# Performance work log

Measured on AMD Instinct MI355X. Metric: run time of the kernel, lower is better.

Reference implementation:

```python
import jax, jax.numpy as jnp
import numpy as np

B, C_IN, C_OUT, RANK, MODES, N = 32, 64, 64, 16, 64, 8192


def setup_inputs() -> dict:
    key = jax.random.key(0)
    k0, k1, k2, k3, k4 = jax.random.split(key, 5)
    x = jax.random.normal(k0, (B, C_IN, N), dtype=jnp.float32)
    U_r = jax.random.normal(k1, (C_IN, RANK), dtype=jnp.float32)
    U_i = jax.random.normal(k2, (C_IN, RANK), dtype=jnp.float32)
    V_r = jax.random.normal(k3, (RANK, C_OUT), dtype=jnp.float32)
    V_i = jax.random.normal(k4, (RANK, C_OUT), dtype=jnp.float32)
    S = jnp.ones((RANK,), dtype=jnp.float32)
    return {"x": x, "U_r": U_r, "U_i": U_i, "V_r": V_r, "V_i": V_i, "S": S}


def reference(x, U_r, U_i, V_r, V_i, S):
    # rFFT over spatial dim, orthonormal normalization (matches torch norm='ortho')
    x_fft = jnp.fft.rfft(x, axis=-1, norm='ortho')          # [B, C_in, N//2+1] complex
    n_freq = x_fft.shape[-1]
    modes = min(MODES, n_freq)
    x_modes = x_fft[..., :modes]                             # [B, C_in, modes]

    U = U_r + 1j * U_i                                       # [C_in, rank]
    V = V_r + 1j * V_i                                       # [rank, C_out]
    # w = (U * S) @ V, then slice first `modes` output channels (as in source)
    w = jnp.einsum('ir,ro->io', U * S[None, :].astype(U.dtype), V)
    w = w[..., :modes]                                       # no-op when C_out == modes

    out_modes = jnp.einsum('bix,io->box', x_modes, w)        # [B, C_out, modes]
    # zero-fill remaining spectrum (equivalent to zeros_like + slice assign)
    full = jnp.pad(out_modes, ((0, 0), (0, 0), (0, n_freq - modes)))
    return jnp.fft.irfft(full, n=x.shape[-1], axis=-1, norm='ortho')
```

## Files before the change

### kernel.cpp

```cpp
#include <hip/hip_runtime.h>

#define NPTS   8192
#define BATCH  32
#define CIN    64
#define COUT   64
#define RANKK  16
#define ROWS   (BATCH * CIN)
#define KB_SPLIT 16

typedef _Float16 f16;
typedef _Float16 f16x4 __attribute__((ext_vector_type(4)));
typedef _Float16 f16x8 __attribute__((ext_vector_type(8)));
typedef float    f32x4 __attribute__((ext_vector_type(4)));

__device__ __forceinline__ void gload16(const void* g, void* l) {
  __builtin_amdgcn_global_load_lds(
      (const __attribute__((address_space(1))) void*)g,
      (__attribute__((address_space(3))) void*)l, 16, 0, 0);
}

__global__ __launch_bounds__(256) void build_tables(f16* __restrict__ T,
                                                    f16* __restrict__ Tt) {
  __shared__ f16 tile[128][18];
  const int n0 = blockIdx.x * 16;
  const int t = threadIdx.x;
#pragma unroll
  for (int j = 0; j < 8; ++j) {
    int flat = t + 256 * j;
    int c = flat >> 4, dn = flat & 15;
    int k = c & 63, n = n0 + dn;
    int m = (k * n) & (NPTS - 1);
    float ang = (float)m * (6.28318530717958647692f / (float)NPTS);
    float sv, cv;
    sincosf(ang, &sv, &cv);
    tile[c][dn] = (f16)((c < 64) ? cv : sv);
  }
  __syncthreads();
#pragma unroll
  for (int j = 0; j < 8; ++j) {
    int flat = t + 256 * j;
    int c = flat >> 4, dn = flat & 15;
    f16 v = tile[c][dn];
    f16 vm = ((c & 1) ? (f16)(-v) : v);
    T[(size_t)c * NPTS + n0 + dn] = v;
    T[(size_t)c * NPTS + n0 + dn + NPTS / 2] = vm;
  }
#pragma unroll
  for (int j = 0; j < 8; ++j) {
    int flat = t + 256 * j;
    int dn = flat >> 7, c = flat & 127;
    f16 v = tile[c][dn];
    f16 vm = ((c & 1) ? (f16)(-v) : v);
    Tt[(size_t)(n0 + dn) * 128 + c] = v;
    Tt[(size_t)(n0 + dn + NPTS / 2) * 128 + c] = vm;
  }
}

__global__ __launch_bounds__(512) void fwd_dft(const float* __restrict__ x,
                                               const f16* __restrict__ T,
                                               f16* __restrict__ Sp) {
  __shared__ __align__(16) char lds[3 * 16384];
  const int t    = threadIdx.x;
  const int w    = t >> 6;
  const int lane = t & 63;
  const int rl = lane & 15, hi = lane >> 4;
  const int kb = blockIdx.x & (KB_SPLIT - 1);
  const int r0 = (blockIdx.x >> 4) * 64;
  const int k0 = kb * (NPTS / KB_SPLIT);

  const int xr_ = t >> 3;
  const int xo_ = ((t & 7) ^ (xr_ & 7)) << 2;
  const int tr_ = t >> 2;
  const int to_ = ((t & 3) ^ (tr_ & 3)) << 3;
  const float* xs0 = x + (size_t)(r0 + xr_) * NPTS + k0 + xo_;
  const f16*   ts0 = T + (size_t)tr_ * NPTS + k0 + to_;
  const int wu = w * 1024;

  auto STAGE = [&](int kt, int slot) {
    char* xb = lds + slot * 16384;
    char* tb = xb + 8192;
    const int kk = kt * 32;
    gload16(xs0 + kk, xb + wu);
    gload16(ts0 + kk, tb + wu);
  };

  f32x4 acc[4];
#pragma unroll
  for (int i = 0; i < 4; ++i) acc[i] = (f32x4){0.f, 0.f, 0.f, 0.f};

  const int h  = w >> 1;
  const int cg = w & 1;
  const int axr = h * 16 + rl;
  const int ad0 = (axr * 8 + ((2 * hi) ^ (axr & 7))) * 16;
  const int ad1 = (axr * 8 + ((2 * hi + 1) ^ (axr & 7))) * 16;
  int bd[4];
#pragma unroll
  for (int s = 0; s < 4; ++s) {
    int trow = cg * 64 + s * 16 + rl;
    bd[s] = (trow * 4 + (hi ^ (trow & 3))) * 16;
  }

  auto COMPUTE = [&](int slot) {
    char* xb = lds + slot * 16384;
    char* tb = xb + 8192;
    f32x4 a0 = *(const f32x4*)(xb + ad0);
    f32x4 a1 = *(const f32x4*)(xb + ad1);
    f16x8 af;
#pragma unroll
    for (int j = 0; j < 4; ++j) { af[j] = (f16)a0[j]; af[4 + j] = (f16)a1[j]; }
#pragma unroll
    for (int s = 0; s < 4; ++s) {
      f16x8 bf = *(const f16x8*)(tb + bd[s]);
      acc[s] = __builtin_amdgcn_mfma_f32_16x16x32_f16(af, bf, acc[s], 0, 0, 0);
    }
  };

  STAGE(0, 0);
  STAGE(1, 1);
  asm volatile("s_waitcnt vmcnt(2)" ::: "memory");
  __builtin_amdgcn_s_barrier();

  int sc = 0, ss = 2;
  for (int kt = 0; kt < 16; ++kt) {
    if (kt + 2 < 16) STAGE(kt + 2, ss);
    COMPUTE(sc);
    if (kt < 15) {
      if (kt + 2 < 16)
        asm volatile("s_waitcnt vmcnt(2)" ::: "memory");
      else
        asm volatile("s_waitcnt vmcnt(0)" ::: "memory");
      __builtin_amdgcn_s_barrier();
    }
    sc = (sc == 2) ? 0 : sc + 1;
    ss = (ss == 2) ? 0 : ss + 1;
  }

  f16* out = Sp + ((size_t)kb * ROWS + r0 + h * 16) * 128 + cg * 64;
#pragma unroll
  for (int s = 0; s < 4; ++s)
#pragma unroll
    for (int i = 0; i < 4; ++i)
      out[(hi * 4 + i) * 128 + s * 16 + rl] = (f16)acc[s][i];
}

__global__ __launch_bounds__(256) void reduce_k(const f16* __restrict__ Sp,
                                                float* __restrict__ Sred) {
  const int idx = blockIdx.x * 256 + threadIdx.x;
  const f16x4* src = (const f16x4*)Sp;
  f32x4 acc = (f32x4){0.f, 0.f, 0.f, 0.f};
#pragma unroll
  for (int s = 0; s < KB_SPLIT; ++s) {
    f16x4 v = src[(size_t)s * (ROWS * 128 / 4) + idx];
#pragma unroll
    for (int e = 0; e < 4; ++e) acc[e] += (float)v[e];
  }
  ((f32x4*)Sred)[idx] = acc;
}

__global__ __launch_bounds__(256) void mix3(const float* __restrict__ Sred,
                                            const float* __restrict__ Ur,
                                            const float* __restrict__ Ui,
                                            const float* __restrict__ Vr,
                                            const float* __restrict__ Vi,
                                            const float* __restrict__ Sv,
                                            f16* __restrict__ Qh) {
  __shared__ float Srs[64][64], Sis[64][64];
  __shared__ float wr_s[64][4], wi_s[64][4];
  const int b  = blockIdx.x >> 4;
  const int og = blockIdx.x & 15;
  const int t  = threadIdx.x;

#pragma unroll
  for (int j = 0; j < 8; ++j) {
    int f4 = t + 256 * j;
    int i = f4 >> 5, kc = (f4 & 31) * 4;
    f32x4 v = *(const f32x4*)(Sred + ((size_t)(b * 64 + i)) * 128 + kc);
    if (kc < 64) *(f32x4*)&Srs[i][kc] = v;
    else         *(f32x4*)&Sis[i][kc - 64] = v;
  }

  {
    int i = t >> 2, ol = t & 3, o = og * 4 + ol;
    float wr = 0.f, wi = 0.f;
#pragma unroll
    for (int r = 0; r < RANKK; ++r) {
      float ur = Ur[i * RANKK + r], ui = Ui[i * RANKK + r];
      float vr = Vr[r * COUT + o],  vi = Vi[r * COUT + o];
      float s = Sv[r];
      wr += s * (ur * vr - ui * vi);
      wi += s * (ur * vi + ui * vr);
    }
    wr_s[i][ol] = wr;
    wi_s[i][ol] = wi;
  }
  __syncthreads();

  const int ol = t >> 6, k = t & 63, o = og * 4 + ol;
  float qr = 0.f, qi = 0.f;
#pragma unroll 4
  for (int i = 0; i < 64; ++i) {
    float sr = Srs[i][k], si = Sis[i][k];
    float wr = wr_s[i][ol], wi = wi_s[i][ol];
    qr += sr * wr + si * wi;
    qi += sr * wi - si * wr;
  }
  float sk = (k == 0 ? 1.0f : 2.0f) / (float)NPTS;
  f16* qrow = Qh + ((size_t)(b * 64 + o)) * 128;
  qrow[k]      = (f16)(qr * sk);
  qrow[64 + k] = (f16)(-qi * sk);
}

__global__ __launch_bounds__(256) void inv_dft(const f16* __restrict__ Qh,
                                               const f16* __restrict__ Tt,
                                               float* __restrict__ y) {
  __shared__ f16   Bt[64][136];
  __shared__ float Tr[4][16][68];
  const int t = threadIdx.x, w = t >> 6, lane = t & 63;
  const int rl = lane & 15, hi = lane >> 4;
  const int nb = blockIdx.x & 127;
  const int rb = blockIdx.x >> 7;
  const int n0 = nb * 64, r0 = rb * 64;

  f16x8 stg[4];
#pragma unroll
  for (int j = 0; j < 4; ++j) {
    int d = j * 256 + t, row = d >> 4, q = d & 15;
    stg[j] = *(const f16x8*)(Tt + (size_t)(n0 + row) * 128 + q * 8);
  }
  const f16* qrow = Qh + (size_t)(r0 + w * 16 + rl) * 128 + 8 * hi;
  f16x8 af[4];
#pragma unroll
  for (int ksv = 0; ksv < 4; ++ksv) af[ksv] = *(const f16x8*)(qrow + ksv * 32);
#pragma unroll
  for (int j = 0; j < 4; ++j) {
    int d = j * 256 + t, row = d >> 4, q = d & 15;
    *(f16x8*)(&Bt[row][q * 8]) = stg[j];
  }
  __syncthreads();

  f32x4 acc[4];
#pragma unroll
  for (int i = 0; i < 4; ++i) acc[i] = (f32x4){0.f, 0.f, 0.f, 0.f};

#pragma unroll
  for (int ksv = 0; ksv < 4; ++ksv)
#pragma unroll
    for (int s = 0; s < 4; ++s) {
      f16x8 bf = *(const f16x8*)(&Bt[s * 16 + rl][(ksv * 4 + hi) * 8]);
      acc[s] = __builtin_amdgcn_mfma_f32_16x16x32_f16(af[ksv], bf, acc[s], 0, 0, 0);
    }

#pragma unroll
  for (int s = 0; s < 4; ++s)
#pragma unroll
    for (int i = 0; i < 4; ++i)
      Tr[w][hi * 4 + i][s * 16 + rl] = acc[s][i];
#pragma unroll
  for (int p = 0; p < 4; ++p) {
    int r = p * 4 + hi;
    f32x4 v = *(const f32x4*)(&Tr[w][r][rl * 4]);
    *(f32x4*)(y + (size_t)(r0 + w * 16 + r) * NPTS + n0 + rl * 4) = v;
  }
}

extern "C" void kernel_launch(void* const* d_in, const int* in_sizes, int n_in,
                              void* d_out, int out_size, void* d_ws, size_t ws_size,
                              hipStream_t stream) {
  const float* x  = (const float*)d_in[0];
  const float* Ur = (const float*)d_in[1];
  const float* Ui = (const float*)d_in[2];
  const float* Vr = (const float*)d_in[3];
  const float* Vi = (const float*)d_in[4];
  const float* Sv = (const float*)d_in[5];
  float* y = (float*)d_out;
  char* ws = (char*)d_ws;

  f16*   T    = (f16*)ws;
  f16*   Tt   = (f16*)(ws + (2u << 20));
  f16*   Sp   = (f16*)(ws + (4u << 20));
  char*  p    = ws + (4u << 20) + (size_t)KB_SPLIT * ROWS * 128 * 2;
  float* Sred = (float*)p;
  f16*   Qh   = (f16*)(p + (size_t)ROWS * 128 * 4);

  build_tables<<<NPTS / 32, 256, 0, stream>>>(T, Tt);
  fwd_dft<<<(ROWS / 64) * KB_SPLIT, 512, 0, stream>>>(x, T, Sp);
  reduce_k<<<ROWS * 128 / 4 / 256, 256, 0, stream>>>(Sp, Sred);
  mix3<<<BATCH * 16, 256, 0, stream>>>(Sred, Ur, Ui, Vr, Vi, Sv, Qh);
  inv_dft<<<(ROWS / 64) * (NPTS / 64), 256, 0, stream>>>(Qh, Tt, y);
}
```

Baseline: 50.19 us.

## Compute DFT twiddle factors on the fly instead of precomputed tables

Removes the build_tables kernel and the global T/Tt twiddle tables. Both the forward and inverse DFT kernels now compute cos/sin values inline with __cosf (sine obtained through a phase offset) and write them straight into LDS. This saves one kernel launch and the table reads and writes from global memory, in exchange for transcendental ALU work inside the pipelined loops. __cosf may be less accurate than sincosf, though the values are rounded to fp16 anyway.

```diff
diff --git a/kernel.cpp b/kernel.cpp
--- a/kernel.cpp
+++ b/kernel.cpp
@@ -13,51 +13,20 @@
 typedef _Float16 f16x8 __attribute__((ext_vector_type(8)));
 typedef float    f32x4 __attribute__((ext_vector_type(4)));
 
+#define TWO_PI_OVER_N (6.28318530717958647692f / (float)NPTS)
+
 __device__ __forceinline__ void gload16(const void* g, void* l) {
   __builtin_amdgcn_global_load_lds(
       (const __attribute__((address_space(1))) void*)g,
       (__attribute__((address_space(3))) void*)l, 16, 0, 0);
 }
 
-__global__ __launch_bounds__(256) void build_tables(f16* __restrict__ T,
-                                                    f16* __restrict__ Tt) {
-  __shared__ f16 tile[128][18];
-  const int n0 = blockIdx.x * 16;
-  const int t = threadIdx.x;
-#pragma unroll
-  for (int j = 0; j < 8; ++j) {
-    int flat = t + 256 * j;
-    int c = flat >> 4, dn = flat & 15;
-    int k = c & 63, n = n0 + dn;
-    int m = (k * n) & (NPTS - 1);
-    float ang = (float)m * (6.28318530717958647692f / (float)NPTS);
-    float sv, cv;
-    sincosf(ang, &sv, &cv);
-    tile[c][dn] = (f16)((c < 64) ? cv : sv);
-  }
-  __syncthreads();
-#pragma unroll
-  for (int j = 0; j < 8; ++j) {
-    int flat = t + 256 * j;
-    int c = flat >> 4, dn = flat & 15;
-    f16 v = tile[c][dn];
-    f16 vm = ((c & 1) ? (f16)(-v) : v);
-    T[(size_t)c * NPTS + n0 + dn] = v;
-    T[(size_t)c * NPTS + n0 + dn + NPTS / 2] = vm;
-  }
-#pragma unroll
-  for (int j = 0; j < 8; ++j) {
-    int flat = t + 256 * j;
-    int dn = flat >> 7, c = flat & 127;
-    f16 v = tile[c][dn];
-    f16 vm = ((c & 1) ? (f16)(-v) : v);
-    Tt[(size_t)(n0 + dn) * 128 + c] = v;
-    Tt[(size_t)(n0 + dn + NPTS / 2) * 128 + c] = vm;
-  }
+__device__ __forceinline__ f16 trig_elem(int freq, int phase_off, int n) {
+  int m = (freq * n + phase_off) & (NPTS - 1);
+  return (f16)__cosf((float)m * TWO_PI_OVER_N);
 }
 
 __global__ __launch_bounds__(512) void fwd_dft(const float* __restrict__ x,
-                                               const f16* __restrict__ T,
                                                f16* __restrict__ Sp) {
   __shared__ __align__(16) char lds[3 * 16384];
   const int t    = threadIdx.x;
@@ -70,18 +39,24 @@
 
   const int xr_ = t >> 3;
   const int xo_ = ((t & 7) ^ (xr_ & 7)) << 2;
-  const int tr_ = t >> 2;
-  const int to_ = ((t & 3) ^ (tr_ & 3)) << 3;
   const float* xs0 = x + (size_t)(r0 + xr_) * NPTS + k0 + xo_;
-  const f16*   ts0 = T + (size_t)tr_ * NPTS + k0 + to_;
   const int wu = w * 1024;
 
-  auto STAGE = [&](int kt, int slot) {
-    char* xb = lds + slot * 16384;
-    char* tb = xb + 8192;
-    const int kk = kt * 32;
-    gload16(xs0 + kk, xb + wu);
-    gload16(ts0 + kk, tb + wu);
+  const int ttrow = t >> 2, tcc = t & 3;
+  const int tg   = tcc ^ (ttrow & 3);
+  const int tfreq = ttrow & 63;
+  const int tpo   = (ttrow < 64) ? 0 : 6144;
+
+  auto STAGE_X = [&](int kt, int slot) {
+    gload16(xs0 + kt * 32, lds + slot * 16384 + wu);
+  };
+  auto STAGE_T = [&](int kt, int slot) {
+    char* tb = lds + slot * 16384 + 8192;
+    const int nb = k0 + kt * 32 + tg * 8;
+    f16x8 v;
+#pragma unroll
+    for (int e = 0; e < 8; ++e) v[e] = trig_elem(tfreq, tpo, nb + e);
+    *(f16x8*)(tb + t * 16) = v;
   };
 
   f32x4 acc[4];
@@ -115,20 +90,20 @@
     }
   };
 
-  STAGE(0, 0);
-  STAGE(1, 1);
-  asm volatile("s_waitcnt vmcnt(2)" ::: "memory");
+  STAGE_X(0, 0); STAGE_T(0, 0);
+  STAGE_X(1, 1); STAGE_T(1, 1);
+  asm volatile("s_waitcnt vmcnt(1) lgkmcnt(0)" ::: "memory");
   __builtin_amdgcn_s_barrier();
 
   int sc = 0, ss = 2;
   for (int kt = 0; kt < 16; ++kt) {
-    if (kt + 2 < 16) STAGE(kt + 2, ss);
+    if (kt + 2 < 16) { STAGE_X(kt + 2, ss); STAGE_T(kt + 2, ss); }
     COMPUTE(sc);
     if (kt < 15) {
       if (kt + 2 < 16)
-        asm volatile("s_waitcnt vmcnt(2)" ::: "memory");
+        asm volatile("s_waitcnt vmcnt(1) lgkmcnt(0)" ::: "memory");
       else
-        asm volatile("s_waitcnt vmcnt(0)" ::: "memory");
+        asm volatile("s_waitcnt vmcnt(0) lgkmcnt(0)" ::: "memory");
       __builtin_amdgcn_s_barrier();
     }
     sc = (sc == 2) ? 0 : sc + 1;
@@ -211,7 +186,6 @@
 }
 
 __global__ __launch_bounds__(256) void inv_dft(const f16* __restrict__ Qh,
-                                               const f16* __restrict__ Tt,
                                                float* __restrict__ y) {
   __shared__ f16   Bt[64][136];
   __shared__ float Tr[4][16][68];
@@ -221,20 +195,21 @@
   const int rb = blockIdx.x >> 7;
   const int n0 = nb * 64, r0 = rb * 64;
 
-  f16x8 stg[4];
+  const f16* qrow = Qh + (size_t)(r0 + w * 16 + rl) * 128 + 8 * hi;
+  f16x8 af[4];
+#pragma unroll
+  for (int ksv = 0; ksv < 4; ++ksv) af[ksv] = *(const f16x8*)(qrow + ksv * 32);
+
 #pragma unroll
   for (int j = 0; j < 4; ++j) {
     int d = j * 256 + t, row = d >> 4, q = d & 15;
-    stg[j] = *(const f16x8*)(Tt + (size_t)(n0 + row) * 128 + q * 8);
-  }
-  const f16* qrow = Qh + (size_t)(r0 + w * 16 + rl) * 128 + 8 * hi;
-  f16x8 af[4];
-#pragma unroll
-  for (int ksv = 0; ksv < 4; ++ksv) af[ksv] = *(const f16x8*)(qrow + ksv * 32);
-#pragma unroll
-  for (int j = 0; j < 4; ++j) {
-    int d = j * 256 + t, row = d >> 4, q = d & 15;
-    *(f16x8*)(&Bt[row][q * 8]) = stg[j];
+    int nn = n0 + row;
+    int freq0 = (q & 7) * 8;
+    int po = (q < 8) ? 0 : 6144;
+    f16x8 v;
+#pragma unroll
+    for (int e = 0; e < 8; ++e) v[e] = trig_elem(freq0 + e, po, nn);
+    *(f16x8*)(&Bt[row][q * 8]) = v;
   }
   __syncthreads();
 
@@ -275,16 +250,13 @@
   float* y = (float*)d_out;
   char* ws = (char*)d_ws;
 
-  f16*   T    = (f16*)ws;
-  f16*   Tt   = (f16*)(ws + (2u << 20));
-  f16*   Sp   = (f16*)(ws + (4u << 20));
-  char*  p    = ws + (4u << 20) + (size_t)KB_SPLIT * ROWS * 128 * 2;
+  f16*   Sp   = (f16*)ws;
+  char*  p    = ws + (size_t)KB_SPLIT * ROWS * 128 * 2;
   float* Sred = (float*)p;
   f16*   Qh   = (f16*)(p + (size_t)ROWS * 128 * 4);
 
-  build_tables<<<NPTS / 32, 256, 0, stream>>>(T, Tt);
-  fwd_dft<<<(ROWS / 64) * KB_SPLIT, 512, 0, stream>>>(x, T, Sp);
+  fwd_dft<<<(ROWS / 64) * KB_SPLIT, 512, 0, stream>>>(x, Sp);
   reduce_k<<<ROWS * 128 / 4 / 256, 256, 0, stream>>>(Sp, Sred);
   mix3<<<BATCH * 16, 256, 0, stream>>>(Sred, Ur, Ui, Vr, Vi, Sv, Qh);
-  inv_dft<<<(ROWS / 64) * (NPTS / 64), 256, 0, stream>>>(Qh, Tt, y);
-}
+  inv_dft<<<(ROWS / 64) * (NPTS / 64), 256, 0, stream>>>(Qh, y);
+}
```

New measurement: 49.55 us. About the same (-1.3%).
